# Kernel optimization log

Measured on AMD Instinct MI355X. Metric: run time of the kernel, lower is better.

The kernel has to match this reference:

```python
import jax, jax.numpy as jnp
import numpy as np

EPS = 1e-12  # torch F.normalize eps

def l2norm(x, axis):
    n = jnp.sqrt(jnp.sum(x * x, axis=axis, keepdims=True))
    return x / jnp.maximum(n, EPS)

def setup_inputs() -> dict:
    key = jax.random.key(0)
    k1, k2, k3, k4 = jax.random.split(key, 4)
    N, C, H, W, K = 128, 128, 64, 64, 64
    x = jax.random.normal(k1, (N, C, H, W), dtype=jnp.float32)
    conv_w = jax.random.normal(k2, (K, C), dtype=jnp.float32) * 0.1
    conv_b = jax.random.normal(k3, (K,), dtype=jnp.float32) * 0.1
    centroids = jax.random.uniform(k4, (K, C), dtype=jnp.float32)
    return {"x": x, "conv_w": conv_w, "conv_b": conv_b, "centroids": centroids}

def reference(x, conv_w, conv_b, centroids):
    N, C, H, W = x.shape
    K = centroids.shape[0]
    xf = x.reshape(N, C, H * W)               # [N, C, S]
    xf = l2norm(xf, axis=1)                   # normalize_input over channels
    # 1x1 conv -> logits [N, K, S], softmax over clusters
    logits = jnp.einsum('ncs,kc->nks', xf, conv_w) + conv_b[None, :, None]
    a = jax.nn.softmax(logits, axis=1)        # [N, K, S]
    # VLAD: sum_s a[n,k,s]*(x[n,:,s] - c[k]) = (a @ x^T) - (sum_s a) * c
    vlad = jnp.einsum('nks,ncs->nkc', a, xf) - a.sum(axis=-1)[:, :, None] * centroids[None]
    vlad = l2norm(vlad, axis=2)               # intra-normalization
    vlad = vlad.reshape(N, K * C)
    return l2norm(vlad, axis=1)
```

## Files before the change

kernel.cpp:

```cpp
#include <hip/hip_runtime.h>
#include <math.h>

#define N_IMG 128
#define C_DIM 128
#define K_CL  64
#define S_PIX 4096
#define PB    8
#define SPB   (S_PIX/PB)
#define CHK   32
#define NCHK  (SPB/CHK)
#define NBUF  4

typedef __attribute__((ext_vector_type(8))) short bf16x8;
typedef __attribute__((ext_vector_type(4))) float f32x4;

__device__ __forceinline__ unsigned short f2bf_rn(float v) {
    unsigned u = __float_as_uint(v);
    unsigned r = u + 0x7fffu + ((u >> 16) & 1u);
    return (unsigned short)(r >> 16);
}
__device__ __forceinline__ float bf2f(unsigned short h) {
    return __uint_as_float(((unsigned)h) << 16);
}

__device__ __forceinline__ int sx(int c) { return ((c & 3) | ((c & 1) << 2)) & 7; }
__device__ __forceinline__ int sa(int k) { return (k >> 2) & 3; }

__device__ __forceinline__ void cvt8(const float* v, bf16x8& h, bf16x8& l) {
    union { unsigned w[4]; bf16x8 v8; } H, L;
    #pragma unroll
    for (int p = 0; p < 4; ++p) {
        unsigned u0 = __float_as_uint(v[2*p]);
        unsigned u1 = __float_as_uint(v[2*p+1]);
        float r0 = v[2*p]   - __uint_as_float(u0 & 0xffff0000u);
        float r1 = v[2*p+1] - __uint_as_float(u1 & 0xffff0000u);
        H.w[p] = __builtin_amdgcn_perm(u1, u0, 0x07060302u);
        L.w[p] = __builtin_amdgcn_perm(__float_as_uint(r1), __float_as_uint(r0), 0x07060302u);
    }
    h = H.v8; l = L.v8;
}

__device__ __forceinline__ void gll16(const float* g, float* l) {
    __builtin_amdgcn_global_load_lds(
        (const __attribute__((address_space(1))) unsigned int*)(g),
        (__attribute__((address_space(3))) unsigned int*)(l),
        16, 0, 0);
}

__global__ void k_prep(const float* __restrict__ w, unsigned short* __restrict__ wf) {
    int i = blockIdx.x * 256 + threadIdx.x;
    int j = i & 7, l = (i >> 3) & 63, t = (i >> 9) & 3, m = (i >> 11) & 3;
    int k = 16*m + (l & 15);
    int c = 32*t + 4*j + (l >> 4);
    float v = w[k * C_DIM + c];
    unsigned short h = f2bf_rn(v);
    wf[i]        = h;
    wf[8192 + i] = f2bf_rn(v - bf2f(h));
}

__global__ void k_clear(float4* __restrict__ out4, float4* __restrict__ asum4) {
    int i = blockIdx.x * 256 + threadIdx.x;
    f32x4 z = (f32x4)0.f;
    if (i < (N_IMG*K_CL*C_DIM)/4) out4[i] = *(float4*)&z;
    if (i < (N_IMG*K_CL)/4)       asum4[i] = *(float4*)&z;
}

__global__ __launch_bounds__(256, 2)
void k_main(const float* __restrict__ x,
            const unsigned short* __restrict__ wf,
            const float* __restrict__ bias,
            float* __restrict__ vlad,
            float* __restrict__ asum)
{
    __shared__ float Xs[NBUF][C_DIM*CHK];
    __shared__ unsigned short aS[2*K_CL*CHK];
    __shared__ float redS[2][2][16];

    const int tid  = threadIdx.x;
    const int lane = tid & 63;
    const int wid  = tid >> 6;
    const int lc   = lane & 15;
    const int g    = lane >> 4;

    const int p  = wid & 1;
    const int mh = wid >> 1;
    const int px = p*16 + lc;
    const int cq = wid * 32;

    const int n  = blockIdx.x / PB;
    const int sp = blockIdx.x % PB;
    const float* xn = x + (size_t)n * (C_DIM * S_PIX) + sp * SPB;

    bf16x8 Wh[2][4], Wl[2][4];
    #pragma unroll
    for (int mm = 0; mm < 2; ++mm)
        #pragma unroll
        for (int t = 0; t < 4; ++t) {
            int m = 2*mh + mm;
            Wh[mm][t] = *(const bf16x8*)&wf[((m*4 + t)*64 + lane)*8];
            Wl[mm][t] = *(const bf16x8*)&wf[((16 + m*4 + t)*64 + lane)*8];
        }
    #pragma unroll
    for (int mm = 0; mm < 2; ++mm)
        #pragma unroll
        for (int t = 0; t < 4; ++t) {
            asm volatile("" : "+v"(Wh[mm][t]));
            asm volatile("" : "+v"(Wl[mm][t]));
        }
    f32x4 bias_r[2];
    #pragma unroll
    for (int mm = 0; mm < 2; ++mm)
        bias_r[mm] = *(const f32x4*)&bias[32*mh + 16*mm + 4*g];

    f32x4 accV[4][2];
    #pragma unroll
    for (int m = 0; m < 4; ++m) { accV[m][0] = (f32x4)0.f; accV[m][1] = (f32x4)0.f; }
    float asum_acc[8];
    #pragma unroll
    for (int i = 0; i < 8; ++i) asum_acc[i] = 0.f;

    const int eA  = g*32 + (((px >> 2) ^ sx(g)) << 2) + (px & 3);
    const int sxB = sx(lc);
    const int saB = sa(lc);

    auto STAGE = [&](int t, float* Xbuf) {
        #pragma unroll
        for (int i2 = 0; i2 < 4; ++i2) {
            int rowblk = wid*32 + i2*8;
            int row = rowblk + (lane >> 3);
            const float* gp = xn + (size_t)row * S_PIX + t*CHK
                            + 4*((lane & 7) ^ sx(row));
            gll16(gp, &Xbuf[rowblk * 32]);
        }
    };

    STAGE(0, Xs[0]);
    STAGE(1, Xs[1]);
    STAGE(2, Xs[2]);
    asm volatile("s_waitcnt vmcnt(8)" ::: "memory");
    __builtin_amdgcn_s_barrier();
    __builtin_amdgcn_sched_barrier(0);

    for (int ch = 0; ch < NCHK; ++ch) {
        float* Xb = Xs[ch & (NBUF-1)];

        if (ch + 3 < NCHK) STAGE(ch + 3, Xs[(ch + 3) & (NBUF-1)]);

        float ss = 0.f;
        f32x4 accL[2];
        accL[0] = (f32x4)0.f; accL[1] = (f32x4)0.f;
        #pragma unroll
        for (int t = 0; t < 4; ++t) {
            float xv[8];
            #pragma unroll
            for (int j = 0; j < 8; ++j)
                xv[j] = Xb[eA + 1024*t + 128*j];
            #pragma unroll
            for (int j = 0; j < 8; ++j) ss = fmaf(xv[j], xv[j], ss);
            bf16x8 xh, xl;
            cvt8(xv, xh, xl);
            #pragma unroll
            for (int mm = 0; mm < 2; ++mm) {
                accL[mm] = __builtin_amdgcn_mfma_f32_16x16x32_bf16(Wh[mm][t], xh, accL[mm], 0,0,0);
                accL[mm] = __builtin_amdgcn_mfma_f32_16x16x32_bf16(Wh[mm][t], xl, accL[mm], 0,0,0);
                accL[mm] = __builtin_amdgcn_mfma_f32_16x16x32_bf16(Wl[mm][t], xh, accL[mm], 0,0,0);
            }
        }
        ss += __shfl_xor(ss, 16); ss += __shfl_xor(ss, 32);
        float rnorm = 1.0f / fmaxf(sqrtf(ss), 1e-12f);

        float e[8]; float sm = 0.f;
        #pragma unroll
        for (int mm = 0; mm < 2; ++mm)
            #pragma unroll
            for (int jj = 0; jj < 4; ++jj) {
                float t2 = __expf(fmaf(accL[mm][jj], rnorm, bias_r[mm][jj]));
                e[mm*4+jj] = t2;
                sm += t2;
            }
        sm += __shfl_xor(sm, 16); sm += __shfl_xor(sm, 32);
        if (g == 0) redS[p][mh][lc] = sm;

        asm volatile("s_waitcnt lgkmcnt(0)" ::: "memory");
        __builtin_amdgcn_s_barrier();
        __builtin_amdgcn_sched_barrier(0);

        float S = sm + redS[p][mh^1][lc];
        float coef  = 1.0f / S;
        float coefr = coef * rnorm;

        #pragma unroll
        for (int mm = 0; mm < 2; ++mm)
            #pragma unroll
            for (int jj = 0; jj < 4; ++jj) {
                float ev = e[mm*4+jj];
                asum_acc[mm*4+jj] += ev * coef;
                float ap = ev * coefr;
                unsigned u = __float_as_uint(ap);
                float r = ap - __uint_as_float(u & 0xffff0000u);
                int k  = 32*mh + 16*mm + 4*g + jj;
                int ix = k*32 + (((px >> 3) ^ g) << 3) + (px & 7);
                aS[ix]        = (unsigned short)(u >> 16);
                aS[2048 + ix] = (unsigned short)(__float_as_uint(r) >> 16);
            }

        asm volatile("s_waitcnt lgkmcnt(0)" ::: "memory");
        __builtin_amdgcn_s_barrier();
        __builtin_amdgcn_sched_barrier(0);

        {
            bf16x8 Ah[4], Al[4];
            #pragma unroll
            for (int m = 0; m < 4; ++m) {
                int off = (16*m + lc)*32 + ((g ^ saB) << 3);
                Ah[m] = *(const bf16x8*)&aS[off];
                Al[m] = *(const bf16x8*)&aS[2048 + off];
            }
            #pragma unroll
            for (int nn = 0; nn < 2; ++nn) {
                int c  = cq + nn*16 + lc;
                int P0 = (2*g) ^ sxB;
                float4 f0 = *(const float4*)&Xb[c*32 + P0*4];
                float4 f1 = *(const float4*)&Xb[c*32 + (P0 ^ 1)*4];
                float xv[8] = {f0.x,f0.y,f0.z,f0.w,f1.x,f1.y,f1.z,f1.w};
                bf16x8 xh, xl;
                cvt8(xv, xh, xl);
                #pragma unroll
                for (int m = 0; m < 4; ++m) {
                    accV[m][nn] = __builtin_amdgcn_mfma_f32_16x16x32_bf16(Ah[m], xh, accV[m][nn], 0,0,0);
                    accV[m][nn] = __builtin_amdgcn_mfma_f32_16x16x32_bf16(Ah[m], xl, accV[m][nn], 0,0,0);
                    accV[m][nn] = __builtin_amdgcn_mfma_f32_16x16x32_bf16(Al[m], xh, accV[m][nn], 0,0,0);
                }
            }
        }

        if (ch + 1 < NCHK) {
            if (ch + 3 < NCHK)
                asm volatile("s_waitcnt vmcnt(8) lgkmcnt(0)" ::: "memory");
            else if (ch + 2 < NCHK)
                asm volatile("s_waitcnt vmcnt(4) lgkmcnt(0)" ::: "memory");
            else
                asm volatile("s_waitcnt vmcnt(0) lgkmcnt(0)" ::: "memory");
            __builtin_amdgcn_s_barrier();
            __builtin_amdgcn_sched_barrier(0);
        }
    }

    float* vb = vlad + (size_t)n * (K_CL * C_DIM);
    #pragma unroll
    for (int m = 0; m < 4; ++m)
        #pragma unroll
        for (int nn = 0; nn < 2; ++nn)
            #pragma unroll
            for (int jj = 0; jj < 4; ++jj)
                atomicAdd(&vb[(16*m + 4*g + jj)*C_DIM + cq + nn*16 + lc],
                          accV[m][nn][jj]);

    #pragma unroll
    for (int i = 0; i < 8; ++i) {
        float v = asum_acc[i];
        v += __shfl_xor(v, 1); v += __shfl_xor(v, 2);
        v += __shfl_xor(v, 4); v += __shfl_xor(v, 8);
        asum_acc[i] = v;
    }
    if (lc == 0) {
        #pragma unroll
        for (int mm = 0; mm < 2; ++mm)
            #pragma unroll
            for (int jj = 0; jj < 4; ++jj)
                atomicAdd(&asum[n*K_CL + 32*mh + 16*mm + 4*g + jj], asum_acc[mm*4+jj]);
    }
}

__global__ __launch_bounds__(256)
void k_final(float* __restrict__ vlad,
             const float* __restrict__ asum,
             const float* __restrict__ cent)
{
    __shared__ float v[K_CL * 132];
    __shared__ float red[K_CL][4];
    __shared__ float rin[K_CL];
    __shared__ float rtot_s;
    const int tid = threadIdx.x;
    const int n   = blockIdx.x;
    float* vb = vlad + (size_t)n * (K_CL * C_DIM);
    const float* as = asum + n * K_CL;

    for (int i = tid; i < K_CL*C_DIM; i += 256) {
        int k = i >> 7, c = i & 127;
        v[k*132 + c] = vb[i] - as[k] * cent[i];
    }
    __syncthreads();
    {
        int k = tid >> 2, p = tid & 3;
        float s2 = 0.f;
        #pragma unroll
        for (int u = 0; u < 32; ++u) { float t = v[k*132 + (u<<2) + p]; s2 = fmaf(t, t, s2); }
        red[k][p] = s2;
    }
    __syncthreads();
    if (tid < K_CL) {
        float s2 = red[tid][0] + red[tid][1] + red[tid][2] + red[tid][3];
        float r  = 1.0f / fmaxf(sqrtf(s2), 1e-12f);
        rin[tid] = r;
        red[tid][0] = s2 * r * r;
    }
    __syncthreads();
    if (tid < 64) {
        float t = red[tid][0];
        t += __shfl_xor(t, 32); t += __shfl_xor(t, 16); t += __shfl_xor(t, 8);
        t += __shfl_xor(t, 4);  t += __shfl_xor(t, 2);  t += __shfl_xor(t, 1);
        if (tid == 0) rtot_s = 1.0f / fmaxf(sqrtf(t), 1e-12f);
    }
    __syncthreads();
    float rt = rtot_s;
    for (int i = tid; i < K_CL*C_DIM; i += 256) {
        vb[i] = v[(i>>7)*132 + (i&127)] * rin[i>>7] * rt;
    }
}

extern "C" void kernel_launch(void* const* d_in, const int* in_sizes, int n_in,
                              void* d_out, int out_size, void* d_ws, size_t ws_size,
                              hipStream_t stream) {
    const float* x    = (const float*)d_in[0];
    const float* w    = (const float*)d_in[1];
    const float* b    = (const float*)d_in[2];
    const float* cent = (const float*)d_in[3];
    float* out = (float*)d_out;
    unsigned short* wf = (unsigned short*)d_ws;
    float* asum = (float*)((char*)d_ws + 32768);

    k_clear<<<(N_IMG*K_CL*C_DIM/4 + 255)/256, 256, 0, stream>>>(
        (float4*)out, (float4*)asum);
    k_prep<<<32, 256, 0, stream>>>(w, wf);
    k_main<<<N_IMG * PB, 256, 0, stream>>>(x, wf, b, out, asum);
    k_final<<<N_IMG, 256, 0, stream>>>(out, asum, cent);
}
```

Before: 115.2 us.

## Remove softmax-sum barrier by folding normalizer into X operand; merge prep kernels

```diff
diff --git a/kernel.cpp b/kernel.cpp
--- a/kernel.cpp
+++ b/kernel.cpp
@@ -47,25 +47,24 @@
         16, 0, 0);
 }
 
-__global__ void k_prep(const float* __restrict__ w, unsigned short* __restrict__ wf) {
-    int i = blockIdx.x * 256 + threadIdx.x;
-    int j = i & 7, l = (i >> 3) & 63, t = (i >> 9) & 3, m = (i >> 11) & 3;
-    int k = 16*m + (l & 15);
-    int c = 32*t + 4*j + (l >> 4);
-    float v = w[k * C_DIM + c];
-    unsigned short h = f2bf_rn(v);
-    wf[i]        = h;
-    wf[8192 + i] = f2bf_rn(v - bf2f(h));
-}
-
-__global__ void k_clear(float4* __restrict__ out4, float4* __restrict__ asum4) {
+__global__ void k_prep(const float* __restrict__ w, unsigned short* __restrict__ wf,
+                       float4* __restrict__ out4, float4* __restrict__ asum4) {
     int i = blockIdx.x * 256 + threadIdx.x;
     f32x4 z = (f32x4)0.f;
     if (i < (N_IMG*K_CL*C_DIM)/4) out4[i] = *(float4*)&z;
     if (i < (N_IMG*K_CL)/4)       asum4[i] = *(float4*)&z;
-}
-
-__global__ __launch_bounds__(256, 2)
+    if (i < 8192) {
+        int j = i & 7, l = (i >> 3) & 63, t = (i >> 9) & 3, m = (i >> 11) & 3;
+        int k = 16*m + (l & 15);
+        int c = 32*t + 4*j + (l >> 4);
+        float v = w[k * C_DIM + c];
+        unsigned short h = f2bf_rn(v);
+        wf[i]        = h;
+        wf[8192 + i] = f2bf_rn(v - bf2f(h));
+    }
+}
+
+__global__ __launch_bounds__(256, 1)
 void k_main(const float* __restrict__ x,
             const unsigned short* __restrict__ wf,
             const float* __restrict__ bias,
@@ -74,7 +73,7 @@
 {
     __shared__ float Xs[NBUF][C_DIM*CHK];
     __shared__ unsigned short aS[2*K_CL*CHK];
-    __shared__ float redS[2][2][16];
+    __shared__ __align__(16) float redS[2][2][16];
 
     const int tid  = threadIdx.x;
     const int lane = tid & 63;
@@ -122,6 +121,8 @@
     const int eA  = g*32 + (((px >> 2) ^ sx(g)) << 2) + (px & 3);
     const int sxB = sx(lc);
     const int saB = sa(lc);
+    const int ps  = g >> 1;
+    const int sb  = (8*g) & 15;
 
     auto STAGE = [&](int t, float* Xbuf) {
         #pragma unroll
@@ -181,21 +182,11 @@
         sm += __shfl_xor(sm, 16); sm += __shfl_xor(sm, 32);
         if (g == 0) redS[p][mh][lc] = sm;
 
-        asm volatile("s_waitcnt lgkmcnt(0)" ::: "memory");
-        __builtin_amdgcn_s_barrier();
-        __builtin_amdgcn_sched_barrier(0);
-
-        float S = sm + redS[p][mh^1][lc];
-        float coef  = 1.0f / S;
-        float coefr = coef * rnorm;
-
         #pragma unroll
         for (int mm = 0; mm < 2; ++mm)
             #pragma unroll
             for (int jj = 0; jj < 4; ++jj) {
-                float ev = e[mm*4+jj];
-                asum_acc[mm*4+jj] += ev * coef;
-                float ap = ev * coefr;
+                float ap = e[mm*4+jj] * rnorm;
                 unsigned u = __float_as_uint(ap);
                 float r = ap - __uint_as_float(u & 0xffff0000u);
                 int k  = 32*mh + 16*mm + 4*g + jj;
@@ -209,6 +200,22 @@
         __builtin_amdgcn_sched_barrier(0);
 
         {
+            float S = sm + redS[p][mh^1][lc];
+            float coef = __builtin_amdgcn_rcpf(S);
+            #pragma unroll
+            for (int i = 0; i < 8; ++i) asum_acc[i] = fmaf(e[i], coef, asum_acc[i]);
+        }
+
+        {
+            float4 u0 = *(const float4*)&redS[ps][0][sb];
+            float4 u1 = *(const float4*)&redS[ps][0][sb+4];
+            float4 v0 = *(const float4*)&redS[ps][1][sb];
+            float4 v1 = *(const float4*)&redS[ps][1][sb+4];
+            float cf[8] = {u0.x+v0.x, u0.y+v0.y, u0.z+v0.z, u0.w+v0.w,
+                           u1.x+v1.x, u1.y+v1.y, u1.z+v1.z, u1.w+v1.w};
+            #pragma unroll
+            for (int j = 0; j < 8; ++j) cf[j] = __builtin_amdgcn_rcpf(cf[j]);
+
             bf16x8 Ah[4], Al[4];
             #pragma unroll
             for (int m = 0; m < 4; ++m) {
@@ -222,7 +229,8 @@
                 int P0 = (2*g) ^ sxB;
                 float4 f0 = *(const float4*)&Xb[c*32 + P0*4];
                 float4 f1 = *(const float4*)&Xb[c*32 + (P0 ^ 1)*4];
-                float xv[8] = {f0.x,f0.y,f0.z,f0.w,f1.x,f1.y,f1.z,f1.w};
+                float xv[8] = {f0.x*cf[0], f0.y*cf[1], f0.z*cf[2], f0.w*cf[3],
+                               f1.x*cf[4], f1.y*cf[5], f1.z*cf[6], f1.w*cf[7]};
                 bf16x8 xh, xl;
                 cvt8(xv, xh, xl);
                 #pragma unroll
@@ -330,9 +338,8 @@
     unsigned short* wf = (unsigned short*)d_ws;
     float* asum = (float*)((char*)d_ws + 32768);
 
-    k_clear<<<(N_IMG*K_CL*C_DIM/4 + 255)/256, 256, 0, stream>>>(
-        (float4*)out, (float4*)asum);
-    k_prep<<<32, 256, 0, stream>>>(w, wf);
+    k_prep<<<(N_IMG*K_CL*C_DIM/4 + 255)/256, 256, 0, stream>>>(
+        w, wf, (float4*)out, (float4*)asum);
     k_main<<<N_IMG * PB, 256, 0, stream>>>(x, wf, b, out, asum);
     k_final<<<N_IMG, 256, 0, stream>>>(out, asum, cent);
 }
```

After: 110.9 us. 1.04x faster.
